# Kernel tuning notes

Measured on AMD Instinct MI355X. Metric: run time of the kernel, lower is better.

The kernel has to match this reference:

```python
import jax, jax.numpy as jnp
import numpy as np

# Fixed Gauss-Legendre quadrature on [-A, A] replacing scipy.integrate.quadrature
A = 5.0
NQ = 64
_x, _w = np.polynomial.legendre.leggauss(NQ)
GL_X = jnp.asarray(_x * A, dtype=jnp.float32)  # nodes scaled to [-5, 5]
# Fold exp(-z^2/2)/sqrt(2*pi) and interval scaling into the weights
GL_W_EFF = jnp.asarray(_w * A * np.exp(-(_x * A) ** 2 / 2.0) / np.sqrt(2.0 * np.pi), dtype=jnp.float32)

# given_params=True constants
SIG_M1, SIG_M2, SIG_I = 1.0, 1.0, 1.0
SIG_M1N1, SIG_M2N2 = 1.0, 0.5
SIG_N1I, SIG_N2I = 0.5, 1.9
SIG_M1W, SIG_M2W = 2.8, -2.2
TAU, DT = 100.0, 20.0


def setup_inputs() -> dict:
    key = jax.random.key(0)
    B, T = 8192, 2048
    u = jax.random.normal(key, (B, T), dtype=jnp.float32)
    return {"u": u}


def reference(u):
    B, T = u.shape
    alpha = jnp.float32(DT / TAU)

    def step(carry, u_t):
        k1, k2, v = carry  # each [B]
        delta = jnp.sqrt(SIG_M1**2 * k1**2 + SIG_M2**2 * k2**2 + SIG_I**2 * u_t**2)  # [B]
        # gauss_int[b] = int_{-A}^{A} (1 - tanh(delta_b z)^2) exp(-z^2/2) dz / sqrt(2pi)
        dphi = 1.0 - jnp.tanh(delta[:, None] * GL_X[None, :]) ** 2  # [B, NQ]
        gauss_int = dphi @ GL_W_EFF  # [B]
        k1_new = k1 + (-k1 + SIG_M1N1 * gauss_int * k1 + SIG_N1I * gauss_int * v) * alpha
        k2_new = k2 + (-k2 + SIG_M2N2 * gauss_int * k2 + SIG_N2I * gauss_int * v) * alpha
        v_new = v + (-v + u_t) * alpha
        z = SIG_M1W * k1_new + SIG_M2W * k2_new
        return (k1_new, k2_new, v_new), z

    zeros = jnp.zeros((B,), dtype=u.dtype)
    _, z_seq = jax.lax.scan(step, (zeros, zeros, zeros), u.T)  # z_seq: [T, B]
    # z_hist: [B, T+1], column 0 is the zero initial state
    z_hist = jnp.concatenate([zeros[:, None], z_seq.T], axis=1)
    return z_hist
```

## Files before the change

### kernel.cpp

```cpp
#include <hip/hip_runtime.h>
#include <math.h>


#define Bsz   8192
#define Tlen  2048
#define TP1   2049
#define NQ    64
#define NG    2049
#define NTAB2 2048
#define INV_H 32.0f
#define CHUNKS 16
#define CLEN  128
#define WARM  128
#define BLOCK 256
#define SIM_GRID 512

#define WS_TAB 128

__global__ __launch_bounds__(256) void setup_kernel(float* __restrict__ ws,
                                                    float* __restrict__ out) {
    __shared__ float  fx[NQ], fw[NQ];
    __shared__ double inv[NQ + 1];
    const int tid = threadIdx.x;
    if (tid <= NQ) inv[tid] = (tid == 0) ? 0.0 : 1.0 / (double)tid;
    __syncthreads();
    if (tid < NQ) {
        double z = cos(3.14159265358979323846 * (tid + 0.75) / (NQ + 0.5));
        double p1 = 1.0, p2 = 0.0, pp = 1.0;
        for (int it = 0; it < 4; ++it) {
            p1 = 1.0; p2 = 0.0;
            for (int j = 1; j <= NQ; ++j) {
                double p3 = p2; p2 = p1;
                p1 = ((2.0 * j - 1.0) * z * p2 - (j - 1.0) * p3) * inv[j];
            }
            pp = NQ * (z * p1 - p2) / (z * z - 1.0);
            if (it < 3) z -= p1 / pp;
        }
        double w  = 2.0 / ((1.0 - z * z) * pp * pp);
        double xs = z * 5.0;
        fx[tid] = (float)xs;
        fw[tid] = (float)(w * 5.0 * exp(-0.5 * xs * xs) * 0.3989422804014327);
    }
    __syncthreads();
    const int j = blockIdx.x * BLOCK + tid;
    if (j < NG) {
        const float d = sqrtf((float)j * (1.0f / INV_H));
        float acc = 0.0f;
        #pragma unroll 8
        for (int q = 0; q < NQ; ++q) {
            float t = tanhf(d * fx[q]);
            acc = fmaf(fw[q], 1.0f - t * t, acc);
        }
        ws[WS_TAB + j] = acc;
    }
    out[(size_t)j * TP1] = 0.0f;
}

__device__ __forceinline__ float step_one(float uu, float& k1, float& k2,
                                          float& v, const float2* s_tab) {
    float s   = fmaf(k1, k1, fmaf(k2, k2, uu * uu));
    float idx = fminf(s * INV_H, 2046.999f);
    int   i0  = (int)idx;
    float f   = idx - (float)i0;
    float2 g2 = s_tab[i0];
    float g   = fmaf(f, g2.y - g2.x, g2.x);
    float gv  = g * v;
    float nk1 = fmaf(k1, fmaf(0.2f, g, 0.8f), 0.10f * gv);
    float nk2 = fmaf(k2, fmaf(0.1f, g, 0.8f), 0.38f * gv);
    v  = fmaf(0.2f, uu - v, v);
    k1 = nk1; k2 = nk2;
    return fmaf(2.8f, nk1, -2.2f * nk2);
}

__global__ __launch_bounds__(BLOCK, 3) void sim_kernel(const float* __restrict__ u,
                                                       const float* __restrict__ ws,
                                                       float* __restrict__ out) {
    __shared__ float2 s_tab[NTAB2];
    __shared__ float2 s_u2[4][BLOCK];
    __shared__ float  s_zt[64 * 65];
    const int tid = threadIdx.x;

    {
        const float* g = ws + WS_TAB;
        #pragma unroll
        for (int i = 0; i < NTAB2 / (BLOCK * 4); ++i) {
            int k = (i * BLOCK + tid) * 4;
            float4 a = *(const float4*)(g + k);
            float  b = g[k + 4];
            s_tab[k + 0] = make_float2(a.x, a.y);
            s_tab[k + 1] = make_float2(a.y, a.z);
            s_tab[k + 2] = make_float2(a.z, a.w);
            s_tab[k + 3] = make_float2(a.w, b);
        }
    }

    const int c    = blockIdx.x >> 5;
    const int bb   = blockIdx.x & 31;
    const int rowb = bb * BLOCK;
    const int t_out   = c * CLEN;
    const int t_begin = (c == 0) ? 0 : (t_out - WARM);

    float k1 = 0.f, k2 = 0.f, v = 0.f;
    const int r1 = tid >> 1;
    const int h4 = (tid & 1) * 4;
    const int ph = (tid & 1) * 2;
    const float* __restrict__ upb = u + (size_t)(rowb + r1) * Tlen + h4;

    float4 Ua = *(const float4*)(upb + t_begin);
    float4 Ub = *(const float4*)(upb + t_begin + 128 * Tlen);

    for (int tb = t_begin; tb < t_out; tb += 8) {
        __syncthreads();
        s_u2[ph    ][r1      ] = make_float2(Ua.x, Ua.y);
        s_u2[ph + 1][r1      ] = make_float2(Ua.z, Ua.w);
        s_u2[ph    ][r1 + 128] = make_float2(Ub.x, Ub.y);
        s_u2[ph + 1][r1 + 128] = make_float2(Ub.z, Ub.w);
        const int tn = tb + 8;
        Ua = *(const float4*)(upb + tn);
        Ub = *(const float4*)(upb + tn + 128 * Tlen);
        __syncthreads();
        #pragma unroll
        for (int p = 0; p < 4; ++p) {
            float2 uu = s_u2[p][tid];
            step_one(uu.x, k1, k2, v, s_tab);
            step_one(uu.y, k1, k2, v, s_tab);
        }
    }

    const int myw = tid >> 6;
    const int lr  = tid & 63;
    for (int h = 0; h < 2; ++h) {
        float zz[64];
        #pragma unroll
        for (int gq = 0; gq < 8; ++gq) {
            const int tb = t_out + h * 64 + gq * 8;
            __syncthreads();
            s_u2[ph    ][r1      ] = make_float2(Ua.x, Ua.y);
            s_u2[ph + 1][r1      ] = make_float2(Ua.z, Ua.w);
            s_u2[ph    ][r1 + 128] = make_float2(Ub.x, Ub.y);
            s_u2[ph + 1][r1 + 128] = make_float2(Ub.z, Ub.w);
            int tn = tb + 8;
            if (tn > Tlen - 8) tn = Tlen - 8;
            Ua = *(const float4*)(upb + tn);
            Ub = *(const float4*)(upb + tn + 128 * Tlen);
            __syncthreads();
            #pragma unroll
            for (int p = 0; p < 4; ++p) {
                float2 uu = s_u2[p][tid];
                zz[gq * 8 + 2 * p    ] = step_one(uu.x, k1, k2, v, s_tab);
                zz[gq * 8 + 2 * p + 1] = step_one(uu.y, k1, k2, v, s_tab);
            }
        }
        const int cb = t_out + 1 + h * 64;
        for (int p4 = 0; p4 < 4; ++p4) {
            __syncthreads();
            if (myw == p4) {
                #pragma unroll
                for (int j = 0; j < 64; ++j)
                    s_zt[lr * 65 + j] = zz[j];
            }
            __syncthreads();
            #pragma unroll
            for (int k = 0; k < 16; ++k) {
                int d   = tid + 256 * k;
                int row = d >> 6;
                int col = d & 63;
                out[(size_t)(rowb + p4 * 64 + row) * TP1 + cb + col] =
                    s_zt[row * 65 + col];
            }
        }
    }
}

extern "C" void kernel_launch(void* const* d_in, const int* in_sizes, int n_in,
                              void* d_out, int out_size, void* d_ws, size_t ws_size,
                              hipStream_t stream) {
    const float* u = (const float*)d_in[0];
    float* out = (float*)d_out;
    float* ws  = (float*)d_ws;
    setup_kernel<<<32, BLOCK, 0, stream>>>(ws, out);
    sim_kernel<<<SIM_GRID, BLOCK, 0, stream>>>(u, ws, out);
}
```

Before: 151.9 us.

## Halve chunk length to double grid, overlay shared buffers, deepen u prefetch

```diff
diff --git a/kernel.cpp b/kernel.cpp
--- a/kernel.cpp
+++ b/kernel.cpp
@@ -9,11 +9,11 @@
 #define NG    2049
 #define NTAB2 2048
 #define INV_H 32.0f
-#define CHUNKS 16
-#define CLEN  128
+#define CHUNKS 32
+#define CLEN  64
 #define WARM  128
 #define BLOCK 256
-#define SIM_GRID 512
+#define SIM_GRID (32 * CHUNKS)
 
 #define WS_TAB 128
 
@@ -72,13 +72,30 @@
     return fmaf(2.8f, nk1, -2.2f * nk2);
 }
 
-__global__ __launch_bounds__(BLOCK, 3) void sim_kernel(const float* __restrict__ u,
+__global__ __launch_bounds__(BLOCK, 4) void sim_kernel(const float* __restrict__ u,
                                                        const float* __restrict__ ws,
                                                        float* __restrict__ out) {
     __shared__ float2 s_tab[NTAB2];
-    __shared__ float2 s_u2[4][BLOCK];
-    __shared__ float  s_zt[64 * 65];
+    __shared__ __align__(16) float s_ovl[64 * 65];
+    float2 (*s_u2)[BLOCK] = (float2 (*)[BLOCK])s_ovl;
+    float* s_zt = s_ovl;
     const int tid = threadIdx.x;
+
+    const int c    = blockIdx.x >> 5;
+    const int bb   = blockIdx.x & 31;
+    const int rowb = bb * BLOCK;
+    const int t_out   = c * CLEN;
+    const int t_begin = (t_out >= WARM) ? (t_out - WARM) : 0;
+
+    const int r1 = tid >> 1;
+    const int h4 = (tid & 1) * 4;
+    const int ph = (tid & 1) * 2;
+    const float* __restrict__ upb = u + (size_t)(rowb + r1) * Tlen + h4;
+
+    float4 Ua0 = *(const float4*)(upb + t_begin);
+    float4 Ub0 = *(const float4*)(upb + t_begin + 128 * Tlen);
+    float4 Ua1 = *(const float4*)(upb + t_begin + 8);
+    float4 Ub1 = *(const float4*)(upb + t_begin + 8 + 128 * Tlen);
 
     {
         const float* g = ws + WS_TAB;
@@ -94,30 +111,18 @@
         }
     }
 
-    const int c    = blockIdx.x >> 5;
-    const int bb   = blockIdx.x & 31;
-    const int rowb = bb * BLOCK;
-    const int t_out   = c * CLEN;
-    const int t_begin = (c == 0) ? 0 : (t_out - WARM);
-
     float k1 = 0.f, k2 = 0.f, v = 0.f;
-    const int r1 = tid >> 1;
-    const int h4 = (tid & 1) * 4;
-    const int ph = (tid & 1) * 2;
-    const float* __restrict__ upb = u + (size_t)(rowb + r1) * Tlen + h4;
-
-    float4 Ua = *(const float4*)(upb + t_begin);
-    float4 Ub = *(const float4*)(upb + t_begin + 128 * Tlen);
 
     for (int tb = t_begin; tb < t_out; tb += 8) {
         __syncthreads();
-        s_u2[ph    ][r1      ] = make_float2(Ua.x, Ua.y);
-        s_u2[ph + 1][r1      ] = make_float2(Ua.z, Ua.w);
-        s_u2[ph    ][r1 + 128] = make_float2(Ub.x, Ub.y);
-        s_u2[ph + 1][r1 + 128] = make_float2(Ub.z, Ub.w);
-        const int tn = tb + 8;
-        Ua = *(const float4*)(upb + tn);
-        Ub = *(const float4*)(upb + tn + 128 * Tlen);
+        s_u2[ph    ][r1      ] = make_float2(Ua0.x, Ua0.y);
+        s_u2[ph + 1][r1      ] = make_float2(Ua0.z, Ua0.w);
+        s_u2[ph    ][r1 + 128] = make_float2(Ub0.x, Ub0.y);
+        s_u2[ph + 1][r1 + 128] = make_float2(Ub0.z, Ub0.w);
+        Ua0 = Ua1; Ub0 = Ub1;
+        const int tn = tb + 16;
+        Ua1 = *(const float4*)(upb + tn);
+        Ub1 = *(const float4*)(upb + tn + 128 * Tlen);
         __syncthreads();
         #pragma unroll
         for (int p = 0; p < 4; ++p) {
@@ -129,45 +134,45 @@
 
     const int myw = tid >> 6;
     const int lr  = tid & 63;
-    for (int h = 0; h < 2; ++h) {
-        float zz[64];
+    float zz[64];
+    #pragma unroll
+    for (int gq = 0; gq < 8; ++gq) {
+        const int tb = t_out + gq * 8;
+        __syncthreads();
+        s_u2[ph    ][r1      ] = make_float2(Ua0.x, Ua0.y);
+        s_u2[ph + 1][r1      ] = make_float2(Ua0.z, Ua0.w);
+        s_u2[ph    ][r1 + 128] = make_float2(Ub0.x, Ub0.y);
+        s_u2[ph + 1][r1 + 128] = make_float2(Ub0.z, Ub0.w);
+        Ua0 = Ua1; Ub0 = Ub1;
+        int tn = tb + 16;
+        if (tn > Tlen - 8) tn = Tlen - 8;
+        Ua1 = *(const float4*)(upb + tn);
+        Ub1 = *(const float4*)(upb + tn + 128 * Tlen);
+        __syncthreads();
         #pragma unroll
-        for (int gq = 0; gq < 8; ++gq) {
-            const int tb = t_out + h * 64 + gq * 8;
-            __syncthreads();
-            s_u2[ph    ][r1      ] = make_float2(Ua.x, Ua.y);
-            s_u2[ph + 1][r1      ] = make_float2(Ua.z, Ua.w);
-            s_u2[ph    ][r1 + 128] = make_float2(Ub.x, Ub.y);
-            s_u2[ph + 1][r1 + 128] = make_float2(Ub.z, Ub.w);
-            int tn = tb + 8;
-            if (tn > Tlen - 8) tn = Tlen - 8;
-            Ua = *(const float4*)(upb + tn);
-            Ub = *(const float4*)(upb + tn + 128 * Tlen);
-            __syncthreads();
+        for (int p = 0; p < 4; ++p) {
+            float2 uu = s_u2[p][tid];
+            zz[gq * 8 + 2 * p    ] = step_one(uu.x, k1, k2, v, s_tab);
+            zz[gq * 8 + 2 * p + 1] = step_one(uu.y, k1, k2, v, s_tab);
+        }
+    }
+
+    const int cb = t_out + 1;
+    for (int p4 = 0; p4 < 4; ++p4) {
+        __syncthreads();
+        if (myw == p4) {
             #pragma unroll
-            for (int p = 0; p < 4; ++p) {
-                float2 uu = s_u2[p][tid];
-                zz[gq * 8 + 2 * p    ] = step_one(uu.x, k1, k2, v, s_tab);
-                zz[gq * 8 + 2 * p + 1] = step_one(uu.y, k1, k2, v, s_tab);
-            }
+            for (int j = 0; j < 64; ++j)
+                s_zt[lr * 65 + j] = zz[j];
         }
-        const int cb = t_out + 1 + h * 64;
-        for (int p4 = 0; p4 < 4; ++p4) {
-            __syncthreads();
-            if (myw == p4) {
-                #pragma unroll
-                for (int j = 0; j < 64; ++j)
-                    s_zt[lr * 65 + j] = zz[j];
-            }
-            __syncthreads();
-            #pragma unroll
-            for (int k = 0; k < 16; ++k) {
-                int d   = tid + 256 * k;
-                int row = d >> 6;
-                int col = d & 63;
-                out[(size_t)(rowb + p4 * 64 + row) * TP1 + cb + col] =
-                    s_zt[row * 65 + col];
-            }
+        __syncthreads();
+        #pragma unroll
+        for (int k = 0; k < 16; ++k) {
+            int d   = tid + 256 * k;
+            int row = d >> 6;
+            int col = d & 63;
+            out[(size_t)(rowb + p4 * 64 + row) * TP1 + cb + col] =
+                s_zt[row * 65 + col];
         }
     }
 }
```

Result: slower. 169.1 us (+11.3%).
